# Optimization experiments

Measured on AMD Instinct MI355X. Metric: run time of the kernel, lower is better.

The kernel has to match this reference:

```python
import jax, jax.numpy as jnp
import numpy as np

NUM_USER = 60000
NUM_ITEM = 40000
DIM = 64
E_U, E_I, E_G = 720000, 480000, 1200000


def _spmm(vals, src, dst, emb, n_rows):
    # sparse.mm(A, emb): out[dst] += A[dst, src] * emb[src]
    return jax.ops.segment_sum(vals[:, None] * emb[src], dst, num_segments=n_rows)


def setup_inputs() -> dict:
    key = jax.random.key(0)
    ks = jax.random.split(key, 11)
    return {
        "users_emb": jax.random.normal(ks[0], (NUM_USER, DIM), dtype=jnp.float32),
        "items_emb": jax.random.normal(ks[1], (NUM_ITEM, DIM), dtype=jnp.float32),
        "user_src": jax.random.randint(ks[2], (E_U,), 0, NUM_USER, dtype=jnp.int32),
        "user_dst": jax.random.randint(ks[3], (E_U,), 0, NUM_USER, dtype=jnp.int32),
        "user_vals": jax.random.uniform(ks[4], (E_U,), dtype=jnp.float32),
        "item_src": jax.random.randint(ks[5], (E_I,), 0, NUM_ITEM, dtype=jnp.int32),
        "item_dst": jax.random.randint(ks[6], (E_I,), 0, NUM_ITEM, dtype=jnp.int32),
        "item_vals": jax.random.uniform(ks[7], (E_I,), dtype=jnp.float32),
        "graph_src": jax.random.randint(ks[8], (E_G,), 0, NUM_USER + NUM_ITEM, dtype=jnp.int32),
        "graph_dst": jax.random.randint(ks[9], (E_G,), 0, NUM_USER + NUM_ITEM, dtype=jnp.int32),
        "graph_vals": jax.random.uniform(ks[10], (E_G,), dtype=jnp.float32),
    }


def reference(users_emb, items_emb, user_src, user_dst, user_vals,
              item_src, item_dst, item_vals, graph_src, graph_dst, graph_vals):
    num_user, num_item = users_emb.shape[0], items_emb.shape[0]
    # h_u1 = sparse.mm(user_mat, users_emb); h_i1 = sparse.mm(item_mat, items_emb)
    h_u1 = _spmm(user_vals, user_src, user_dst, users_emb, num_user)
    h_i1 = _spmm(item_vals, item_src, item_dst, items_emb, num_item)
    # all_emb_tran = sparse.mm(graph, cat([users_emb, items_emb]))  (unused for mode=0)
    all_emb = jnp.concatenate([users_emb, items_emb], axis=0)
    all_tran = _spmm(graph_vals, graph_src, graph_dst, all_emb, num_user + num_item)
    h_u2, h_i2 = all_tran[:num_user], all_tran[num_user:]
    # mode == 0 -> return (h_u1, h_i1)
    return (h_u1, h_i1)
```

## Files before the change

### kernel.cpp

```cpp
#include <hip/hip_runtime.h>
#include <hip/hip_fp16.h>

#define DIM   64
#define TILE  64
#define TSH   6
#define CHUNK 2048
#define ACHUNK 1024
#define ATHREADS 512
#define CAPMARGIN 256

__global__ void __launch_bounds__(256) spmm_edge_kernel(
    const float* __restrict__ vals, const int* __restrict__ src,
    const int* __restrict__ dst, const float* __restrict__ emb,
    float* __restrict__ out, int n_edges)
{
    int e    = blockIdx.x * 4 + (threadIdx.x >> 6);
    int lane = threadIdx.x & 63;
    if (e >= n_edges) return;
    atomicAdd(&out[(size_t)dst[e] * DIM + lane],
              vals[e] * emb[(size_t)src[e] * DIM + lane]);
}

__global__ void __launch_bounds__(1024) scatter_kernel(
    const int* __restrict__ src_u, const int* __restrict__ dst_u,
    const float* __restrict__ val_u, int n_u, int nblk_u,
    const int* __restrict__ src_i, const int* __restrict__ dst_i,
    const float* __restrict__ val_i, int n_i,
    int nbu, int cap_u, int cap_i,
    int* __restrict__ bcur, int2* __restrict__ pay,
    int nblk_edges, int nblk_cvt,
    const float4* __restrict__ cvt_u, const float4* __restrict__ cvt_i,
    __half2* __restrict__ cvt_dst, long n4u, long n4tot)
{
    __shared__ int  lcnt[1024];
    __shared__ int  lscan[1024];
    __shared__ int  gbase[1024];
    __shared__ int  wsum[16];
    __shared__ int2 stage[CHUNK];
    __shared__ int  gidx[CHUNK];

    if ((int)blockIdx.x >= nblk_edges) {
        int cb = blockIdx.x - nblk_edges;
        int t  = threadIdx.x;
        for (long i = (long)cb * 1024 + t; i < n4tot; i += (long)nblk_cvt * 1024) {
            float4 f = (i < n4u) ? cvt_u[i] : cvt_i[i - n4u];
            cvt_dst[2 * i]     = __floats2half2_rn(f.x, f.y);
            cvt_dst[2 * i + 1] = __floats2half2_rn(f.z, f.w);
        }
        return;
    }

    const int* src; const int* dst; const float* vals;
    int n, bucket_base, base, cap, region_base;
    if ((int)blockIdx.x < nblk_u) {
        src = src_u; dst = dst_u; vals = val_u; n = n_u;
        bucket_base = 0;   base = blockIdx.x * CHUNK;
        cap = cap_u; region_base = 0;
    } else {
        src = src_i; dst = dst_i; vals = val_i; n = n_i;
        bucket_base = nbu; base = (blockIdx.x - nblk_u) * CHUNK;
        cap = cap_i; region_base = nbu * cap_u;
    }

    int tid  = threadIdx.x;
    int wid  = tid >> 6;
    int lane = tid & 63;

    lcnt[tid] = 0;
    __syncthreads();

    int pk[2], vb[2], bk[2], tk[2];
    bool ok[2];
#pragma unroll
    for (int k = 0; k < 2; ++k) {
        int i = base + k * 1024 + tid;
        ok[k] = (i < n);
        if (ok[k]) {
            int s = src[i], d = dst[i];
            vb[k] = __float_as_int(vals[i]);
            bk[k] = d >> TSH;
            pk[k] = (s << TSH) | (d & (TILE - 1));
            tk[k] = atomicAdd(&lcnt[bk[k]], 1);
        }
    }
    __syncthreads();

    int c = lcnt[tid];
    int s = c;
#pragma unroll
    for (int d = 1; d < 64; d <<= 1) {
        int u = __shfl_up(s, d, 64);
        if (lane >= d) s += u;
    }
    if (lane == 63) wsum[wid] = s;
    __syncthreads();
    if (wid == 0 && lane < 16) {
        int v  = wsum[lane];
        int t3 = v;
#pragma unroll
        for (int d = 1; d < 16; d <<= 1) {
            int u = __shfl_up(t3, d, 64);
            if (lane >= d) t3 += u;
        }
        wsum[lane] = t3 - v;
    }
    __syncthreads();
    lscan[tid] = s + wsum[wid];
    gbase[tid] = c ? (region_base + tid * cap +
                      atomicAdd(&bcur[bucket_base + tid], c))
                   : 0;
    __syncthreads();

#pragma unroll
    for (int k = 0; k < 2; ++k) {
        if (ok[k]) {
            int b  = bk[k];
            int sp = lscan[b] - lcnt[b] + tk[k];
            stage[sp] = make_int2(pk[k], vb[k]);
            gidx[sp]  = gbase[b] + tk[k];
        }
    }
    __syncthreads();

    int tot = lscan[1023];
    for (int i = tid; i < tot; i += 1024)
        pay[gidx[i]] = stage[i];
}

struct H4 { __half2 a, b; };

__device__ __forceinline__ float4 gld4(const __half* e, int rowelem, int gl) {
    H4 h = *((const H4*)(e + rowelem) + gl);
    float2 fa = __half22float2(h.a), fb = __half22float2(h.b);
    return make_float4(fa.x, fa.y, fb.x, fb.y);
}
__device__ __forceinline__ float4 gld4(const float* e, int rowelem, int gl) {
    return *((const float4*)(e + rowelem) + gl);
}

template <typename ET>
__global__ void __launch_bounds__(ATHREADS) accum_kernel(
    const int2* __restrict__ pay, const int* __restrict__ bcur, int nbu,
    int cap_u, int cap_i,
    const ET* __restrict__ emb_u, const ET* __restrict__ emb_i,
    float* __restrict__ out_u, float* __restrict__ out_i, int nu, int ni)
{
    __shared__ int2 stage[ACHUNK];
    __shared__ int  rs[TILE];
    __shared__ int  rc[TILE];

    int b = blockIdx.x;
    const ET* emb; float* out; int row0, nrows, start;
    if (b < nbu) {
        emb = emb_u; out = out_u; row0 = b << TSH; nrows = nu;
        start = b * cap_u;
    } else {
        emb = emb_i; out = out_i; row0 = (b - nbu) << TSH; nrows = ni;
        start = nbu * cap_u + (b - nbu) * cap_i;
    }
    int end = start + bcur[b];

    int tid  = threadIdx.x;
    int wid  = tid >> 6;
    int lane = tid & 63;
    int g    = lane >> 4;
    int gl   = lane & 15;

    float4 acc[2];
    acc[0] = make_float4(0.f, 0.f, 0.f, 0.f);
    acc[1] = make_float4(0.f, 0.f, 0.f, 0.f);

    for (int cb = start; cb < end; cb += ACHUNK) {
        int cn = end - cb; if (cn > ACHUNK) cn = ACHUNK;

        if (tid < TILE) rc[tid] = 0;
        __syncthreads();

        int2 e[2]; int rl[2], tk[2]; bool ok[2];
#pragma unroll
        for (int k = 0; k < 2; ++k) {
            int i = tid + ATHREADS * k;
            ok[k] = (i < cn);
            if (ok[k]) {
                e[k]  = pay[cb + i];
                rl[k] = e[k].x & (TILE - 1);
                tk[k] = atomicAdd(&rc[rl[k]], 1);
            }
        }
        __syncthreads();

        if (wid == 0) {
            int c = rc[lane];
            int s = c;
#pragma unroll
            for (int d = 1; d < 64; d <<= 1) {
                int t = __shfl_up(s, d, 64);
                if (lane >= d) s += t;
            }
            rs[lane] = s - c;
        }
        __syncthreads();

#pragma unroll
        for (int k = 0; k < 2; ++k)
            if (ok[k]) stage[rs[rl[k]] + tk[k]] = e[k];
        __syncthreads();

#pragma unroll
        for (int rr = 0; rr < 2; ++rr) {
            int r    = wid * 8 + g * 2 + rr;
            int j    = rs[r];
            int jend = j + rc[r];
            float4 a = acc[rr];
            for (; j + 3 < jend; j += 4) {
                int2 p0 = stage[j], p1 = stage[j + 1], p2 = stage[j + 2], p3 = stage[j + 3];
                float4 g0 = gld4(emb, p0.x & ~(TILE - 1), gl);
                float4 g1 = gld4(emb, p1.x & ~(TILE - 1), gl);
                float4 g2 = gld4(emb, p2.x & ~(TILE - 1), gl);
                float4 g3 = gld4(emb, p3.x & ~(TILE - 1), gl);
                float v0 = __int_as_float(p0.y), v1 = __int_as_float(p1.y);
                float v2 = __int_as_float(p2.y), v3 = __int_as_float(p3.y);
                a.x += v0 * g0.x; a.y += v0 * g0.y; a.z += v0 * g0.z; a.w += v0 * g0.w;
                a.x += v1 * g1.x; a.y += v1 * g1.y; a.z += v1 * g1.z; a.w += v1 * g1.w;
                a.x += v2 * g2.x; a.y += v2 * g2.y; a.z += v2 * g2.z; a.w += v2 * g2.w;
                a.x += v3 * g3.x; a.y += v3 * g3.y; a.z += v3 * g3.z; a.w += v3 * g3.w;
            }
            for (; j < jend; ++j) {
                int2 p = stage[j];
                float4 gg = gld4(emb, p.x & ~(TILE - 1), gl);
                float v = __int_as_float(p.y);
                a.x += v * gg.x; a.y += v * gg.y; a.z += v * gg.z; a.w += v * gg.w;
            }
            acc[rr] = a;
        }
        __syncthreads();
    }

#pragma unroll
    for (int rr = 0; rr < 2; ++rr) {
        int r = row0 + wid * 8 + g * 2 + rr;
        if (r < nrows)
            *((float4*)(out + (size_t)r * DIM) + gl) = acc[rr];
    }
}

extern "C" void kernel_launch(void* const* d_in, const int* in_sizes, int n_in,
                              void* d_out, int out_size, void* d_ws, size_t ws_size,
                              hipStream_t stream)
{
    const float* users_emb = (const float*)d_in[0];
    const float* items_emb = (const float*)d_in[1];
    const int*   user_src  = (const int*)  d_in[2];
    const int*   user_dst  = (const int*)  d_in[3];
    const float* user_vals = (const float*)d_in[4];
    const int*   item_src  = (const int*)  d_in[5];
    const int*   item_dst  = (const int*)  d_in[6];
    const float* item_vals = (const float*)d_in[7];

    const int E_u = in_sizes[2];
    const int E_i = in_sizes[5];
    const int NU  = in_sizes[0] / DIM;
    const int NI  = in_sizes[1] / DIM;

    float* out = (float*)d_out;

    const int NBU = (NU + TILE - 1) / TILE;
    const int NBI = (NI + TILE - 1) / TILE;
    const int NB  = NBU + NBI;

    const int cap_u = (E_u + NBU - 1) / NBU + CAPMARGIN;
    const int cap_i = (E_i + NBI - 1) / NBI + CAPMARGIN;

    size_t hdr_ints    = ((size_t)NB + 1) & ~(size_t)1;
    size_t pay_entries = (size_t)NBU * cap_u + (size_t)NBI * cap_i;
    size_t need_core   = hdr_ints * sizeof(int) + pay_entries * sizeof(int2);
    size_t emb_bytes   = (size_t)(NU + NI) * DIM * sizeof(__half);
    size_t need16      = need_core + emb_bytes;

    if (ws_size < need_core || NU > 65536 || NI > 65536) {
        hipMemsetAsync(d_out, 0, (size_t)out_size * sizeof(float), stream);
        spmm_edge_kernel<<<dim3((E_u + 3) / 4), dim3(256), 0, stream>>>(
            user_vals, user_src, user_dst, users_emb, out, E_u);
        spmm_edge_kernel<<<dim3((E_i + 3) / 4), dim3(256), 0, stream>>>(
            item_vals, item_src, item_dst, items_emb, out + (size_t)NU * DIM, E_i);
        return;
    }

    int*  bcur = (int*)d_ws;
    int2* pay  = (int2*)((int*)d_ws + hdr_ints);

    const bool use_fp16 = (ws_size >= need16);
    __half* embh = (__half*)((char*)d_ws + need_core);

    hipMemsetAsync(bcur, 0, (size_t)NB * sizeof(int), stream);

    const int nblk_u   = (E_u + CHUNK - 1) / CHUNK;
    const int nblk_i   = (E_i + CHUNK - 1) / CHUNK;
    const int nbe      = nblk_u + nblk_i;
    const int nblk_cvt = use_fp16 ? 128 : 0;
    const long n4u     = (long)NU * (DIM / 4);
    const long n4tot   = (long)(NU + NI) * (DIM / 4);

    scatter_kernel<<<dim3(nbe + nblk_cvt), dim3(1024), 0, stream>>>(
        user_src, user_dst, user_vals, E_u, nblk_u,
        item_src, item_dst, item_vals, E_i,
        NBU, cap_u, cap_i, bcur, pay,
        nbe, nblk_cvt,
        (const float4*)users_emb, (const float4*)items_emb,
        (__half2*)embh, n4u, n4tot);

    if (use_fp16) {
        accum_kernel<__half><<<dim3(NB), dim3(ATHREADS), 0, stream>>>(
            pay, bcur, NBU, cap_u, cap_i, embh, embh + (size_t)NU * DIM,
            out, out + (size_t)NU * DIM, NU, NI);
    } else {
        accum_kernel<float><<<dim3(NB), dim3(ATHREADS), 0, stream>>>(
            pay, bcur, NBU, cap_u, cap_i, users_emb, items_emb,
            out, out + (size_t)NU * DIM, NU, NI);
    }
}
```

Baseline: 71.38 us.

## Double-buffer edge staging in accum kernel to prefetch next chunk

The shared-memory staging buffers, row counts and offsets in the accumulation kernel are doubled. While the current chunk of edges is being accumulated, the next chunk's payload is loaded from global memory into registers, then bucketed into the alternate buffer. This is meant to hide payload load latency and cut one barrier per chunk. It doubles the kernel's shared-memory footprint, which may lower occupancy, and it does little when a block holds only one chunk.

```diff
diff --git a/kernel.cpp b/kernel.cpp
--- a/kernel.cpp
+++ b/kernel.cpp
@@ -145,9 +145,9 @@
     const ET* __restrict__ emb_u, const ET* __restrict__ emb_i,
     float* __restrict__ out_u, float* __restrict__ out_i, int nu, int ni)
 {
-    __shared__ int2 stage[ACHUNK];
-    __shared__ int  rs[TILE];
-    __shared__ int  rc[TILE];
+    __shared__ int2 stage[2][ACHUNK];
+    __shared__ int  rs[2][TILE];
+    __shared__ int  rc[2][TILE];
 
     int b = blockIdx.x;
     const ET* emb; float* out; int row0, nrows, start;
@@ -170,50 +170,67 @@
     acc[0] = make_float4(0.f, 0.f, 0.f, 0.f);
     acc[1] = make_float4(0.f, 0.f, 0.f, 0.f);
 
-    for (int cb = start; cb < end; cb += ACHUNK) {
-        int cn = end - cb; if (cn > ACHUNK) cn = ACHUNK;
-
-        if (tid < TILE) rc[tid] = 0;
-        __syncthreads();
-
+    int nch = (end - start + ACHUNK - 1) / ACHUNK;
+
+    if (tid < TILE) { rc[0][tid] = 0; rc[1][tid] = 0; }
+    __syncthreads();
+
+    if (nch > 0) {
+        int cn = end - start; if (cn > ACHUNK) cn = ACHUNK;
         int2 e[2]; int rl[2], tk[2]; bool ok[2];
 #pragma unroll
         for (int k = 0; k < 2; ++k) {
             int i = tid + ATHREADS * k;
             ok[k] = (i < cn);
             if (ok[k]) {
-                e[k]  = pay[cb + i];
+                e[k]  = pay[start + i];
                 rl[k] = e[k].x & (TILE - 1);
-                tk[k] = atomicAdd(&rc[rl[k]], 1);
-            }
-        }
-        __syncthreads();
-
+                tk[k] = atomicAdd(&rc[0][rl[k]], 1);
+            }
+        }
+        __syncthreads();
         if (wid == 0) {
-            int c = rc[lane];
+            int c = rc[0][lane];
             int s = c;
 #pragma unroll
             for (int d = 1; d < 64; d <<= 1) {
                 int t = __shfl_up(s, d, 64);
                 if (lane >= d) s += t;
             }
-            rs[lane] = s - c;
-        }
-        __syncthreads();
-
+            rs[0][lane] = s - c;
+        }
+        __syncthreads();
 #pragma unroll
         for (int k = 0; k < 2; ++k)
-            if (ok[k]) stage[rs[rl[k]] + tk[k]] = e[k];
-        __syncthreads();
-
+            if (ok[k]) stage[0][rs[0][rl[k]] + tk[k]] = e[k];
+        __syncthreads();
+    }
+
+    for (int t = 0; t < nch; ++t) {
+        int cur = t & 1, nxt = cur ^ 1;
+        bool have_next = (t + 1 < nch);
+
+        int2 e[2]; int rl[2], tk[2]; bool ok[2] = { false, false };
+        if (have_next) {
+            int cb_n = start + (t + 1) * ACHUNK;
+            int cn_n = end - cb_n; if (cn_n > ACHUNK) cn_n = ACHUNK;
+#pragma unroll
+            for (int k = 0; k < 2; ++k) {
+                int i = tid + ATHREADS * k;
+                ok[k] = (i < cn_n);
+                if (ok[k]) e[k] = pay[cb_n + i];
+            }
+        }
+
+        const int2* st = stage[cur];
 #pragma unroll
         for (int rr = 0; rr < 2; ++rr) {
             int r    = wid * 8 + g * 2 + rr;
-            int j    = rs[r];
-            int jend = j + rc[r];
+            int j    = rs[cur][r];
+            int jend = j + rc[cur][r];
             float4 a = acc[rr];
             for (; j + 3 < jend; j += 4) {
-                int2 p0 = stage[j], p1 = stage[j + 1], p2 = stage[j + 2], p3 = stage[j + 3];
+                int2 p0 = st[j], p1 = st[j + 1], p2 = st[j + 2], p3 = st[j + 3];
                 float4 g0 = gld4(emb, p0.x & ~(TILE - 1), gl);
                 float4 g1 = gld4(emb, p1.x & ~(TILE - 1), gl);
                 float4 g2 = gld4(emb, p2.x & ~(TILE - 1), gl);
@@ -226,12 +243,44 @@
                 a.x += v3 * g3.x; a.y += v3 * g3.y; a.z += v3 * g3.z; a.w += v3 * g3.w;
             }
             for (; j < jend; ++j) {
-                int2 p = stage[j];
+                int2 p = st[j];
                 float4 gg = gld4(emb, p.x & ~(TILE - 1), gl);
                 float v = __int_as_float(p.y);
                 a.x += v * gg.x; a.y += v * gg.y; a.z += v * gg.z; a.w += v * gg.w;
             }
             acc[rr] = a;
+        }
+
+        if (have_next) {
+#pragma unroll
+            for (int k = 0; k < 2; ++k)
+                if (ok[k]) {
+                    rl[k] = e[k].x & (TILE - 1);
+                    tk[k] = atomicAdd(&rc[nxt][rl[k]], 1);
+                }
+        }
+        __syncthreads();
+
+        if (have_next) {
+            if (wid == 0) {
+                int c = rc[nxt][lane];
+                int s = c;
+#pragma unroll
+                for (int d = 1; d < 64; d <<= 1) {
+                    int t2 = __shfl_up(s, d, 64);
+                    if (lane >= d) s += t2;
+                }
+                rs[nxt][lane] = s - c;
+            } else if (wid == 1) {
+                rc[cur][lane] = 0;
+            }
+        }
+        __syncthreads();
+
+        if (have_next) {
+#pragma unroll
+            for (int k = 0; k < 2; ++k)
+                if (ok[k]) stage[nxt][rs[nxt][rl[k]] + tk[k]] = e[k];
         }
         __syncthreads();
     }
```

Result: no change. 71.69 us (+0.4%).
